# Optimization experiments

Measured on AMD Instinct MI355X. Metric: run time of the kernel, lower is better.

## Reference

```python
import jax, jax.numpy as jnp
import numpy as np

B, S, W, D, H = 2, 2048, 32, 1024, 16

def setup_inputs() -> dict:
    key = jax.random.key(0)
    ks = jax.random.split(key, 8)
    scale = 0.02
    return {
        'q': jax.random.normal(ks[0], (B, S, D), jnp.float32),
        'k': jax.random.normal(ks[1], (B, S, W, D), jnp.float32),
        'v': jax.random.normal(ks[2], (B, S, W, D), jnp.float32),
        'Wq': jax.random.normal(ks[3], (D, D), jnp.float32) * scale,
        'bq': jnp.zeros((D,), jnp.float32),
        'Wk': jax.random.normal(ks[4], (D, D), jnp.float32) * scale,
        'bk': jnp.zeros((D,), jnp.float32),
        'Wv': jax.random.normal(ks[5], (D, D), jnp.float32) * scale,
        'bv': jnp.zeros((D,), jnp.float32),
        'Wo': jax.random.normal(ks[6], (D, D), jnp.float32) * scale,
        'bo': jnp.zeros((D,), jnp.float32),
        'num_heads': H,
    }

def reference(q, k, v, Wq, bq, Wk, bk, Wv, bv, Wo, bo, num_heads):
    b, s, d = q.shape
    w = k.shape[2]
    hd = d // num_heads
    # query: Linear -> view(B,S,H,1,hd) -> transpose(1,2) => (B,H,S,1,hd)
    qh = (q @ Wq.T + bq).reshape(b, s, num_heads, 1, hd).transpose(0, 2, 1, 3, 4)
    # key/value: Linear then RAW view (B,H,S,W,hd) -- faithful to torch .view (no head transpose)
    kh = (k @ Wk.T + bk).reshape(b, num_heads, s, w, hd)
    vh = (v @ Wv.T + bv).reshape(b, num_heads, s, w, hd)
    # scores: (B,H,S,1,W), scaled by sqrt(head_dim) (query.shape[-1] inside attention)
    scores = jnp.einsum('bhsid,bhswd->bhsiw', qh, kh) / jnp.sqrt(jnp.float32(hd))
    # Softmax(dim=1) normalizes over the HEAD axis -- faithful to the original
    attn = jax.nn.softmax(scores, axis=1)
    A = jnp.einsum('bhsiw,bhswd->bhsid', attn, vh)[:, :, :, 0, :]  # (B,H,S,hd)
    out = A.reshape(b, s, d)  # raw view, matches torch .view(B,S,D)
    return out @ Wo.T + bo
```

## Files before the change

kernel.cpp:

```cpp
#include <hip/hip_runtime.h>
#include <hip/hip_bf16.h>


#define DEVI __device__ __forceinline__

typedef __attribute__((ext_vector_type(8))) short bf16x8;
typedef __attribute__((ext_vector_type(4))) float f32x4;
typedef const __attribute__((address_space(1))) void* gvp;
typedef __attribute__((address_space(3))) void* lvp;

DEVI ushort f2bf(float f) {
  uint u = __float_as_uint(f);
  u = u + 0x7fffu + ((u >> 16) & 1u);
  return (ushort)(u >> 16);
}
DEVI float bf2f(ushort u) { return __uint_as_float(((uint)u) << 16); }

__global__ __launch_bounds__(256) void cast_kernel(const float* __restrict__ in,
                                                   ushort* __restrict__ out,
                                                   long n) {
  long i = ((long)blockIdx.x * 256 + threadIdx.x) * 8;
  const long stride = (long)gridDim.x * 256 * 8;
  for (; i < n; i += stride) {
    float4 a = *reinterpret_cast<const float4*>(in + i);
    float4 b = *reinterpret_cast<const float4*>(in + i + 4);
    ushort o[8];
    o[0] = f2bf(a.x); o[1] = f2bf(a.y); o[2] = f2bf(a.z); o[3] = f2bf(a.w);
    o[4] = f2bf(b.x); o[5] = f2bf(b.y); o[6] = f2bf(b.z); o[7] = f2bf(b.w);
    *reinterpret_cast<int4*>(out + i) = *reinterpret_cast<const int4*>(o);
  }
}

template <int FJ0>
DEVI void mfma16b(f32x4 (&acc)[8][4], const bf16x8 (&A)[8], const bf16x8 (&B)[2]) {
  __builtin_amdgcn_s_setprio(1);
#pragma unroll
  for (int fi = 0; fi < 8; ++fi)
#pragma unroll
    for (int j = 0; j < 2; ++j)
      acc[fi][FJ0 + j] = __builtin_amdgcn_mfma_f32_16x16x32_bf16(
          A[fi], B[j], acc[fi][FJ0 + j], 0, 0, 0);
  __builtin_amdgcn_s_setprio(0);
}

__global__ __launch_bounds__(512)
__attribute__((amdgpu_waves_per_eu(2, 2)))
void gemm_big(const float* __restrict__ Ag, const ushort* __restrict__ Wg,
              const float* __restrict__ bias, ushort* __restrict__ Cg) {
  constexpr int K = 1024;
  __shared__ char lds[131072];
  const int tid = threadIdx.x;
  const int lane = tid & 63;
  const int wave = tid >> 6;
  const int wm = wave >> 2;
  const int wn = wave & 3;
  const int d = blockIdx.x;
  const int bn = (d >> 3) & 3;
  const size_t bm = (size_t)(d & 7) * (gridDim.x >> 5) + (d >> 5);

  const ushort* bB = Wg + (size_t)bn * 256 * K;

  const int r0 = tid >> 3;
  const int c0 = (tid & 7) ^ (r0 & 7);
  const float* pR0 = Ag + bm * 256 * K + (size_t)r0 * K + c0 * 8;
  const float* pR1 = pR0 + 64 * K;
  const ushort* bS0 = bB + (size_t)r0 * K + c0 * 8;
  const ushort* bS1 = bB + (size_t)(r0 + 64) * K + c0 * 8;
  const ushort* bS2 = bB + (size_t)(r0 + 128) * K + c0 * 8;
  const ushort* bS3 = bB + (size_t)(r0 + 192) * K + c0 * 8;

  const int lm = lane & 15;
  const int q = lane >> 4;
  const int rowB = lm * 128;
  const int swz0 = (q ^ (lm & 7)) * 16;
  const int swz1 = ((4 + q) ^ (lm & 7)) * 16;
  const char* ldsc = (const char*)lds;
  const char* p0A = ldsc + wm * 16384 + rowB;
  const char* p0B = ldsc + 32768 + (wn >> 1) * 16384 + (wn & 1) * 8192 + rowB;
  const char* p1A = p0A + 65536;
  const char* p1B = p0B + 65536;

  f32x4 acc[8][4] = {};
  bf16x8 A8[8];
  bf16x8 Bf[2];
  float4 st[8];

#define SB0 __builtin_amdgcn_sched_barrier(0)
#define BAR __builtin_amdgcn_s_barrier()
#define STG(p0, p1, ktE, ldsOff)                                                 \
  {                                                                              \
    __builtin_amdgcn_global_load_lds((gvp)((p0) + (ktE)),                        \
                                     (lvp)(lds + (ldsOff) + tid * 16), 16, 0, 0);\
    __builtin_amdgcn_global_load_lds((gvp)((p1) + (ktE)),                        \
                                     (lvp)(lds + (ldsOff) + 8192 + tid * 16),    \
                                     16, 0, 0);                                  \
  }
#define AISS8(off)                                                      \
  {                                                                     \
    st[0] = *reinterpret_cast<const float4*>(pR0 + (off));              \
    st[1] = *reinterpret_cast<const float4*>(pR0 + (off) + 4);          \
    st[2] = *reinterpret_cast<const float4*>(pR1 + (off));              \
    st[3] = *reinterpret_cast<const float4*>(pR1 + (off) + 4);          \
    st[4] = *reinterpret_cast<const float4*>(pR0 + 131072 + (off));     \
    st[5] = *reinterpret_cast<const float4*>(pR0 + 131072 + (off) + 4); \
    st[6] = *reinterpret_cast<const float4*>(pR1 + 131072 + (off));     \
    st[7] = *reinterpret_cast<const float4*>(pR1 + 131072 + (off) + 4); \
  }
#define CVTPAIR(v0, v1, dstoff)                                              \
  {                                                                          \
    uint w0, w1, w2, w3;                                                     \
    asm("v_cvt_pk_bf16_f32 %0,%1,%2" : "=v"(w0) : "v"((v0).x), "v"((v0).y)); \
    asm("v_cvt_pk_bf16_f32 %0,%1,%2" : "=v"(w1) : "v"((v0).z), "v"((v0).w)); \
    asm("v_cvt_pk_bf16_f32 %0,%1,%2" : "=v"(w2) : "v"((v1).x), "v"((v1).y)); \
    asm("v_cvt_pk_bf16_f32 %0,%1,%2" : "=v"(w3) : "v"((v1).z), "v"((v1).w)); \
    *reinterpret_cast<uint4*>(lds + (dstoff) + tid * 16) =                   \
        make_uint4(w0, w1, w2, w3);                                          \
  }
#define CVT8(base)                          \
  {                                         \
    CVTPAIR(st[0], st[1], (base));          \
    CVTPAIR(st[2], st[3], (base) + 8192);   \
    CVTPAIR(st[4], st[5], (base) + 16384);  \
    CVTPAIR(st[6], st[7], (base) + 24576);  \
  }
#define PH_SYNC()                                    \
  __builtin_amdgcn_s_barrier();                      \
  asm volatile("s_waitcnt lgkmcnt(0)" ::: "memory"); \
  SB0;
#define LDA8(p, swz)                                                       \
  _Pragma("unroll") for (int i_ = 0; i_ < 8; ++i_) {                       \
    A8[i_] = *reinterpret_cast<const bf16x8*>((p) + i_ * 2048 + (swz));    \
  }
#define LDB2(p, fjb, swz)                                                  \
  {                                                                        \
    Bf[0] = *reinterpret_cast<const bf16x8*>((p) + (fjb) + (swz));         \
    Bf[1] = *reinterpret_cast<const bf16x8*>((p) + (fjb) + 2048 + (swz));  \
  }

  AISS8(0); SB0;
  CVT8(0);
  SB0;
  STG(bS0, bS1, 0, 32768); STG(bS2, bS3, 0, 49152); SB0;
  AISS8(64); SB0;
  asm volatile("s_waitcnt vmcnt(8)" ::: "memory");
  asm volatile("s_waitcnt lgkmcnt(0)" ::: "memory");
  BAR;
  SB0;

#define ITER(M)                                                           \
  {                                                                       \
    const int ktB1 = (2 * it + 1) * 64;                                   \
    const int ktB2 = (2 * it + 2) * 64;                                   \
    const int ktA2 = (2 * it + 2) * 64;                                   \
    const int ktA3 = (2 * it + 3) * 64;                                   \
              \
    LDA8(p0A, swz0); LDB2(p0B, 0, swz0);                                  \
    STG(bS0, bS1, ktB1, 98304); STG(bS2, bS3, ktB1, 114688);              \
    PH_SYNC(); mfma16b<0>(acc, A8, Bf); BAR;                              \
        \
    LDB2(p0B, 4096, swz0);                                                \
    CVT8(65536);                                                          \
    SB0;                                                                  \
    if (M == 0) { AISS8(ktA2); SB0; }                                     \
    PH_SYNC(); mfma16b<2>(acc, A8, Bf); BAR;                              \
                                                  \
    LDA8(p0A, swz1); LDB2(p0B, 0, swz1);                                  \
    PH_SYNC(); mfma16b<0>(acc, A8, Bf); BAR;                              \
                   \
    LDB2(p0B, 4096, swz1);                                                \
    PH_SYNC(); mfma16b<2>(acc, A8, Bf);                                   \
    SB0;                                                                  \
    if (M == 0) { asm volatile("s_waitcnt vmcnt(8)" ::: "memory"); }      \
    else        { asm volatile("s_waitcnt vmcnt(0)" ::: "memory"); }      \
    BAR; SB0;                                                             \
              \
    LDA8(p1A, swz0); LDB2(p1B, 0, swz0);                                  \
    if (M == 0) { STG(bS0, bS1, ktB2, 32768); STG(bS2, bS3, ktB2, 49152); } \
    PH_SYNC(); mfma16b<0>(acc, A8, Bf); BAR;                              \
        \
    LDB2(p1B, 4096, swz0);                                                \
    if (M == 0) { CVT8(0); SB0; AISS8(ktA3); SB0; }                       \
    PH_SYNC(); mfma16b<2>(acc, A8, Bf); BAR;                              \
                                                  \
    LDA8(p1A, swz1); LDB2(p1B, 0, swz1);                                  \
    PH_SYNC(); mfma16b<0>(acc, A8, Bf); BAR;                              \
                   \
    LDB2(p1B, 4096, swz1);                                                \
    PH_SYNC(); mfma16b<2>(acc, A8, Bf);                                   \
    if (M == 0) {                                                         \
      SB0;                                                                \
      asm volatile("s_waitcnt vmcnt(8)" ::: "memory");                    \
      BAR; SB0;                                                           \
    }                                                                     \
  }

#pragma unroll 1
  for (int it = 0; it < 7; ++it) ITER(0);
  { const int it = 7; ITER(1); }
#undef ITER
#undef STG
#undef AISS8
#undef CVTPAIR
#undef CVT8
#undef PH_SYNC
#undef LDA8
#undef LDB2
#undef SB0
#undef BAR

#pragma unroll
  for (int fi = 0; fi < 8; ++fi) {
#pragma unroll
    for (int fj = 0; fj < 4; ++fj) {
      int n = bn * 256 + wn * 64 + fj * 16 + lm;
      float bv = bias[n];
#pragma unroll
      for (int r = 0; r < 4; ++r) {
        size_t m = bm * 256 + wm * 128 + fi * 16 + ((lane >> 4) * 4) + r;
        Cg[m * 1024 + n] = f2bf(acc[fi][fj][r] + bv);
      }
    }
  }
}

template <typename TOUT>
__global__ __launch_bounds__(256) void gemm_lds(const ushort* __restrict__ Ag,
                                                const ushort* __restrict__ Wg,
                                                const float* __restrict__ bias,
                                                TOUT* __restrict__ Cg) {
  constexpr int K = 1024;
  __shared__ ushort lA[128 * 64];
  __shared__ ushort lB[128 * 64];
  const int tid = threadIdx.x;
  const int lane = tid & 63;
  const int wave = tid >> 6;
  const int wr = (wave >> 1) * 64;
  const int wc = (wave & 1) * 64;
  const int d = blockIdx.x;
  const int bn = (d >> 3) & 7;
  const size_t bm = (size_t)(d & 7) * (gridDim.x >> 6) + (d >> 6);

  const ushort* aB = Ag + bm * 128 * K;
  const ushort* bB = Wg + (size_t)bn * 128 * K;
  const int srow = wave * 32 + (lane >> 3);
  const int scol = ((lane & 7) ^ (lane >> 3)) * 8;
  char* lAc = (char*)lA;
  char* lBc = (char*)lB;

  f32x4 acc[4][4] = {};

  for (int kt = 0; kt < K; kt += 64) {
    __syncthreads();
#pragma unroll
    for (int c = 0; c < 4; ++c) {
      __builtin_amdgcn_global_load_lds(
          (gvp)(aB + (size_t)(srow + c * 8) * K + kt + scol),
          (lvp)(lAc + wave * 4096 + c * 1024), 16, 0, 0);
      __builtin_amdgcn_global_load_lds(
          (gvp)(bB + (size_t)(srow + c * 8) * K + kt + scol),
          (lvp)(lBc + wave * 4096 + c * 1024), 16, 0, 0);
    }
    __syncthreads();
#pragma unroll
    for (int kk = 0; kk < 2; ++kk) {
      bf16x8 af[4], bg[4];
#pragma unroll
      for (int fi = 0; fi < 4; ++fi) {
        int r = wr + fi * 16 + (lane & 15);
        int byte = (r * 128 + kk * 64 + ((lane >> 4) * 16)) ^ ((r & 7) << 4);
        af[fi] = *reinterpret_cast<const bf16x8*>(lAc + byte);
      }
#pragma unroll
      for (int fj = 0; fj < 4; ++fj) {
        int r = wc + fj * 16 + (lane & 15);
        int byte = (r * 128 + kk * 64 + ((lane >> 4) * 16)) ^ ((r & 7) << 4);
        bg[fj] = *reinterpret_cast<const bf16x8*>(lBc + byte);
      }
#pragma unroll
      for (int fi = 0; fi < 4; ++fi)
#pragma unroll
        for (int fj = 0; fj < 4; ++fj)
          acc[fi][fj] = __builtin_amdgcn_mfma_f32_16x16x32_bf16(af[fi], bg[fj],
                                                                acc[fi][fj], 0, 0, 0);
    }
  }
#pragma unroll
  for (int fi = 0; fi < 4; ++fi) {
#pragma unroll
    for (int fj = 0; fj < 4; ++fj) {
      int n = bn * 128 + wc + fj * 16 + (lane & 15);
      float bv = bias[n];
#pragma unroll
      for (int r = 0; r < 4; ++r) {
        size_t m = bm * 128 + wr + fi * 16 + ((lane >> 4) * 4) + r;
        float val = acc[fi][fj][r] + bv;
        if constexpr (sizeof(TOUT) == 2)
          reinterpret_cast<ushort*>(Cg)[m * 1024 + n] = f2bf(val);
        else
          reinterpret_cast<float*>(Cg)[m * 1024 + n] = val;
      }
    }
  }
}

template <typename TIN, typename TOUT>
__global__ __launch_bounds__(256) void gemm_bias(const TIN* __restrict__ Ag,
                                                 const float* __restrict__ Wg,
                                                 const float* __restrict__ bias,
                                                 TOUT* __restrict__ Cg) {
  constexpr int K = 1024;
  __shared__ char lA[128 * 64 * 2];
  __shared__ char lB[128 * 64 * 2];
  const int tid = threadIdx.x;
  const int lane = tid & 63;
  const int wave = tid >> 6;
  const int wr = (wave >> 1) * 64;
  const int wc = (wave & 1) * 64;
  const int bn = blockIdx.x;
  const size_t bm = blockIdx.y;

  const TIN* aBase = Ag + bm * 128 * K;
  const float* bBase = Wg + (size_t)bn * 128 * K;

  f32x4 acc[4][4] = {};

  for (int kt = 0; kt < K; kt += 64) {
    __syncthreads();
    if constexpr (sizeof(TIN) == 4) {
#pragma unroll
      for (int i = 0; i < 8; ++i) {
        int f = tid + i * 256;
        int row = f >> 4, c4 = f & 15;
        const float4 v = *reinterpret_cast<const float4*>(
            reinterpret_cast<const float*>(aBase) + (size_t)row * K + kt + c4 * 4);
        ushort4 pk;
        pk.x = f2bf(v.x); pk.y = f2bf(v.y); pk.z = f2bf(v.z); pk.w = f2bf(v.w);
        int byte = (row * 128 + c4 * 8) ^ ((row & 7) << 4);
        *reinterpret_cast<ushort4*>(lA + byte) = pk;
      }
    } else {
#pragma unroll
      for (int i = 0; i < 4; ++i) {
        int f = tid + i * 256;
        int row = f >> 3, c8 = f & 7;
        int4 v = *reinterpret_cast<const int4*>(
            reinterpret_cast<const ushort*>(aBase) + (size_t)row * K + kt + c8 * 8);
        int byte = (row * 128 + c8 * 16) ^ ((row & 7) << 4);
        *reinterpret_cast<int4*>(lA + byte) = v;
      }
    }
#pragma unroll
    for (int i = 0; i < 8; ++i) {
      int f = tid + i * 256;
      int row = f >> 4, c4 = f & 15;
      const float4 v =
          *reinterpret_cast<const float4*>(bBase + (size_t)row * K + kt + c4 * 4);
      ushort4 pk;
      pk.x = f2bf(v.x); pk.y = f2bf(v.y); pk.z = f2bf(v.z); pk.w = f2bf(v.w);
      int byte = (row * 128 + c4 * 8) ^ ((row & 7) << 4);
      *reinterpret_cast<ushort4*>(lB + byte) = pk;
    }
    __syncthreads();
#pragma unroll
    for (int kk = 0; kk < 2; ++kk) {
      bf16x8 af[4], bg[4];
#pragma unroll
      for (int fi = 0; fi < 4; ++fi) {
        int r = wr + fi * 16 + (lane & 15);
        int byte = (r * 128 + kk * 64 + ((lane >> 4) * 16)) ^ ((r & 7) << 4);
        af[fi] = *reinterpret_cast<const bf16x8*>(lA + byte);
      }
#pragma unroll
      for (int fj = 0; fj < 4; ++fj) {
        int r = wc + fj * 16 + (lane & 15);
        int byte = (r * 128 + kk * 64 + ((lane >> 4) * 16)) ^ ((r & 7) << 4);
        bg[fj] = *reinterpret_cast<const bf16x8*>(lB + byte);
      }
#pragma unroll
      for (int fi = 0; fi < 4; ++fi)
#pragma unroll
        for (int fj = 0; fj < 4; ++fj)
          acc[fi][fj] =
              __builtin_amdgcn_mfma_f32_16x16x32_bf16(af[fi], bg[fj], acc[fi][fj], 0, 0, 0);
    }
  }
#pragma unroll
  for (int fi = 0; fi < 4; ++fi) {
#pragma unroll
    for (int fj = 0; fj < 4; ++fj) {
      int n = bn * 128 + wc + fj * 16 + (lane & 15);
      float bv = bias[n];
#pragma unroll
      for (int r = 0; r < 4; ++r) {
        size_t m = bm * 128 + wr + fi * 16 + ((lane >> 4) * 4) + r;
        float val = acc[fi][fj][r] + bv;
        if constexpr (sizeof(TOUT) == 2)
          reinterpret_cast<ushort*>(Cg)[m * 1024 + n] = f2bf(val);
        else
          reinterpret_cast<float*>(Cg)[m * 1024 + n] = val;
      }
    }
  }
}

__global__ __launch_bounds__(512) void attn_kernel(const ushort* __restrict__ Q,
                                                   const ushort* __restrict__ Kl,
                                                   const ushort* __restrict__ Vl,
                                                   ushort* __restrict__ Aout) {
  const int bs = blockIdx.x;
  const int b = bs >> 11, sp = bs & 2047;
  const int tid = threadIdx.x;
  const int wave = tid >> 6, lane = tid & 63;

  __shared__ ushort qrow[1024];
  __shared__ float sc[16][32];
  __shared__ float attnw[16][32];
  __shared__ float mx[32], rinv[32];

  reinterpret_cast<uint*>(qrow)[tid] =
      reinterpret_cast<const uint*>(Q + (size_t)bs * 1024)[tid];
  __syncthreads();

  const int wp = lane & 31, half = lane >> 5;
#pragma unroll
  for (int hh = 0; hh < 2; ++hh) {
    const int h = wave * 2 + hh;
    const int s_k = h * 128 + (sp >> 4);
    const int w_k = (sp & 15) * 2 + (wp >> 4);
    const ushort* kp =
        Kl + (((size_t)(b * 2048 + s_k) * 32) + w_k) * 1024 + (wp & 15) * 64 + half * 32;
    const ushort* qp = qrow + h * 64 + half * 32;
    float dot = 0.f;
#pragma unroll
    for (int j = 0; j < 32; j += 8) {
      int4 kv = *reinterpret_cast<const int4*>(kp + j);
      int4 qv = *reinterpret_cast<const int4*>(qp + j);
      const ushort* ka = reinterpret_cast<const ushort*>(&kv);
      const ushort* qa = reinterpret_cast<const ushort*>(&qv);
#pragma unroll
      for (int t = 0; t < 8; ++t) dot += bf2f(ka[t]) * bf2f(qa[t]);
    }
    dot += __shfl_xor(dot, 32);
    if (half == 0) sc[h][wp] = dot * 0.125f;
  }
  __syncthreads();
  if (tid < 32) {
    float m = sc[0][tid];
#pragma unroll
    for (int h = 1; h < 16; ++h) m = fmaxf(m, sc[h][tid]);
    float s = 0.f;
#pragma unroll
    for (int h = 0; h < 16; ++h) s += __expf(sc[h][tid] - m);
    mx[tid] = m;
    rinv[tid] = 1.f / s;
  }
  __syncthreads();
  if (lane < 32) {
#pragma unroll
    for (int hh = 0; hh < 2; ++hh) {
      const int h = wave * 2 + hh;
      attnw[h][lane] = __expf(sc[h][lane] - mx[lane]) * rinv[lane];
    }
  }
  __syncthreads();
#pragma unroll
  for (int hh = 0; hh < 2; ++hh) {
    const int h = wave * 2 + hh;
    const int s_k = h * 128 + (sp >> 4);
    const size_t vb = (((size_t)(b * 2048 + s_k) * 32) + (sp & 15) * 2) * 1024;
    float a = 0.f;
#pragma unroll
    for (int w2 = 0; w2 < 32; ++w2) {
      float wgt = attnw[h][w2];
      a += wgt * bf2f(Vl[vb + (size_t)(w2 >> 4) * 1024 + (w2 & 15) * 64 + lane]);
    }
    Aout[(((size_t)(b * 16 + h)) * 2048 + sp) * 64 + lane] = f2bf(a);
  }
}

extern "C" void kernel_launch(void* const* d_in, const int* in_sizes, int n_in,
                              void* d_out, int out_size, void* d_ws, size_t ws_size,
                              hipStream_t stream) {
  const float* q = (const float*)d_in[0];
  const float* k = (const float*)d_in[1];
  const float* v = (const float*)d_in[2];
  const float* Wq = (const float*)d_in[3];
  const float* bq = (const float*)d_in[4];
  const float* Wk = (const float*)d_in[5];
  const float* bk = (const float*)d_in[6];
  const float* Wv = (const float*)d_in[7];
  const float* bv = (const float*)d_in[8];
  const float* Wo = (const float*)d_in[9];
  const float* bo = (const float*)d_in[10];
  float* out = (float*)d_out;

  char* ws = (char*)d_ws;
  const size_t MB = 1u << 20;
  ushort* Qlin = (ushort*)ws;
  ushort* Aws  = (ushort*)(ws + 8 * MB);
  ushort* wkbf = (ushort*)(ws + 16 * MB);
  ushort* wvbf = (ushort*)(ws + 18 * MB);
  ushort* wqbf = (ushort*)(ws + 20 * MB);
  ushort* wobf = (ushort*)(ws + 22 * MB);
  ushort* qbf  = (ushort*)(ws + 24 * MB);
  ushort* Klin = (ushort*)(ws + 32 * MB);
  ushort* Vlin = (ushort*)(ws + 288 * MB);
  const bool full = ws_size >= 800 * MB;

  if (full) {
    cast_kernel<<<dim3(512), 256, 0, stream>>>(Wq, wqbf, 1048576L);
    cast_kernel<<<dim3(512), 256, 0, stream>>>(Wk, wkbf, 1048576L);
    cast_kernel<<<dim3(512), 256, 0, stream>>>(Wv, wvbf, 1048576L);
    cast_kernel<<<dim3(512), 256, 0, stream>>>(Wo, wobf, 1048576L);
    cast_kernel<<<dim3(2048), 256, 0, stream>>>(q, qbf, 4194304L);
    gemm_lds<ushort><<<dim3(256), 256, 0, stream>>>(qbf, wqbf, bq, Qlin);
    gemm_big<<<dim3(2048), 512, 0, stream>>>(k, wkbf, bk, Klin);
    gemm_big<<<dim3(2048), 512, 0, stream>>>(v, wvbf, bv, Vlin);
    attn_kernel<<<dim3(4096), dim3(512), 0, stream>>>(Qlin, Klin, Vlin, Aws);
    gemm_lds<float><<<dim3(256), 256, 0, stream>>>(Aws, wobf, bo, out);
  } else {
    gemm_bias<float, ushort><<<dim3(8, 32), 256, 0, stream>>>(q, Wq, bq, Qlin);
    gemm_bias<float, ushort><<<dim3(8, 1024), 256, 0, stream>>>(k, Wk, bk, Klin);
    gemm_bias<float, ushort><<<dim3(8, 1024), 256, 0, stream>>>(v, Wv, bv, Vlin);
    attn_kernel<<<dim3(4096), dim3(512), 0, stream>>>(Qlin, Klin, Vlin, Aws);
    gemm_bias<ushort, float><<<dim3(8, 32), 256, 0, stream>>>(Aws, Wo, bo, out);
  }
}
```

Baseline: 913.7 us.

## Fuse V fp32-to-bf16 cast into K projection GEMM, add bf16-input V GEMM

The K projection GEMM now also streams the fp32 V tensor, converting it to bf16 in slots between its MFMA phases and writing it to a workspace buffer. A new bf16-input GEMM with a 4-slot global_load_lds pipeline then computes the V projection from that buffer. The aim is to hide V's conversion cost under the compute-bound K GEMM and let the V GEMM read half the bytes. The price is extra bf16 write and read traffic for V, plus added memory and register pressure inside the K GEMM's carefully scheduled loop.

```diff
diff --git a/kernel.cpp b/kernel.cpp
--- a/kernel.cpp
+++ b/kernel.cpp
@@ -45,8 +45,9 @@
 
 __global__ __launch_bounds__(512)
 __attribute__((amdgpu_waves_per_eu(2, 2)))
-void gemm_big(const float* __restrict__ Ag, const ushort* __restrict__ Wg,
-              const float* __restrict__ bias, ushort* __restrict__ Cg) {
+void gemm_big_f32(const float* __restrict__ Ag, const ushort* __restrict__ Wg,
+                  const float* __restrict__ bias, ushort* __restrict__ Cg,
+                  const float* __restrict__ Vsrc, ushort* __restrict__ Vbf) {
   constexpr int K = 1024;
   __shared__ char lds[131072];
   const int tid = threadIdx.x;
@@ -80,10 +81,14 @@
   const char* p1A = p0A + 65536;
   const char* p1B = p0B + 65536;
 
+  const float* rsrc = Vsrc + (size_t)d * 65536 + tid * 4;
+  ushort* rdst = Vbf + (size_t)d * 65536 + tid * 4;
+
   f32x4 acc[8][4] = {};
   bf16x8 A8[8];
   bf16x8 Bf[2];
   float4 st[8];
+  float4 rv;
 
 #define SB0 __builtin_amdgcn_sched_barrier(0)
 #define BAR __builtin_amdgcn_s_barrier()
@@ -136,6 +141,14 @@
     Bf[0] = *reinterpret_cast<const bf16x8*>((p) + (fjb) + (swz));         \
     Bf[1] = *reinterpret_cast<const bf16x8*>((p) + (fjb) + 2048 + (swz));  \
   }
+#define RLD(u) { rv = *reinterpret_cast<const float4*>(rsrc + (size_t)(u) * 2048); }
+#define RST(u)                                                               \
+  {                                                                          \
+    uint w0, w1;                                                             \
+    asm("v_cvt_pk_bf16_f32 %0,%1,%2" : "=v"(w0) : "v"(rv.x), "v"(rv.y));     \
+    asm("v_cvt_pk_bf16_f32 %0,%1,%2" : "=v"(w1) : "v"(rv.z), "v"(rv.w));     \
+    *reinterpret_cast<uint2*>(rdst + (size_t)(u) * 2048) = make_uint2(w0, w1);\
+  }
 
   AISS8(0); SB0;
   CVT8(0);
@@ -156,18 +169,22 @@
               \
     LDA8(p0A, swz0); LDB2(p0B, 0, swz0);                                  \
     STG(bS0, bS1, ktB1, 98304); STG(bS2, bS3, ktB1, 114688);              \
+    RLD(it * 4 + 0);                                                      \
     PH_SYNC(); mfma16b<0>(acc, A8, Bf); BAR;                              \
         \
     LDB2(p0B, 4096, swz0);                                                \
     CVT8(65536);                                                          \
     SB0;                                                                  \
     if (M == 0) { AISS8(ktA2); SB0; }                                     \
+    RST(it * 4 + 0);                                                      \
     PH_SYNC(); mfma16b<2>(acc, A8, Bf); BAR;                              \
                                                   \
     LDA8(p0A, swz1); LDB2(p0B, 0, swz1);                                  \
+    RLD(it * 4 + 1);                                                      \
     PH_SYNC(); mfma16b<0>(acc, A8, Bf); BAR;                              \
                    \
     LDB2(p0B, 4096, swz1);                                                \
+    RST(it * 4 + 1);                                                      \
     PH_SYNC(); mfma16b<2>(acc, A8, Bf);                                   \
     SB0;                                                                  \
     if (M == 0) { asm volatile("s_waitcnt vmcnt(8)" ::: "memory"); }      \
@@ -176,16 +193,20 @@
               \
     LDA8(p1A, swz0); LDB2(p1B, 0, swz0);                                  \
     if (M == 0) { STG(bS0, bS1, ktB2, 32768); STG(bS2, bS3, ktB2, 49152); } \
+    RLD(it * 4 + 2);                                                      \
     PH_SYNC(); mfma16b<0>(acc, A8, Bf); BAR;                              \
         \
     LDB2(p1B, 4096, swz0);                                                \
     if (M == 0) { CVT8(0); SB0; AISS8(ktA3); SB0; }                       \
+    RST(it * 4 + 2);                                                      \
     PH_SYNC(); mfma16b<2>(acc, A8, Bf); BAR;                              \
                                                   \
     LDA8(p1A, swz1); LDB2(p1B, 0, swz1);                                  \
+    RLD(it * 4 + 3);                                                      \
     PH_SYNC(); mfma16b<0>(acc, A8, Bf); BAR;                              \
                    \
     LDB2(p1B, 4096, swz1);                                                \
+    RST(it * 4 + 3);                                                      \
     PH_SYNC(); mfma16b<2>(acc, A8, Bf);                                   \
     if (M == 0) {                                                         \
       SB0;                                                                \
@@ -205,8 +226,120 @@
 #undef PH_SYNC
 #undef LDA8
 #undef LDB2
+#undef RLD
+#undef RST
 #undef SB0
 #undef BAR
+
+#pragma unroll
+  for (int fi = 0; fi < 8; ++fi) {
+#pragma unroll
+    for (int fj = 0; fj < 4; ++fj) {
+      int n = bn * 256 + wn * 64 + fj * 16 + lm;
+      float bv = bias[n];
+#pragma unroll
+      for (int r = 0; r < 4; ++r) {
+        size_t m = bm * 256 + wm * 128 + fi * 16 + ((lane >> 4) * 4) + r;
+        Cg[m * 1024 + n] = f2bf(acc[fi][fj][r] + bv);
+      }
+    }
+  }
+}
+
+__global__ __launch_bounds__(512, 2) void gemm_big_bf16(const ushort* __restrict__ Ag,
+                                                        const ushort* __restrict__ Wg,
+                                                        const float* __restrict__ bias,
+                                                        ushort* __restrict__ Cg) {
+  constexpr int K = 1024;
+  constexpr int NT = 32;
+  constexpr int SLOT = 32768;
+  __shared__ char lds[4 * SLOT];
+  const int tid = threadIdx.x;
+  const int lane = tid & 63;
+  const int wave = tid >> 6;
+  const int wm = wave >> 2;
+  const int wn = wave & 3;
+  const int d = blockIdx.x;
+  const int bn = (d >> 3) & 3;
+  const size_t bm = (size_t)(d & 7) * (gridDim.x >> 5) + (d >> 5);
+
+  const ushort* aB = Ag + bm * 256 * K;
+  const ushort* bB = Wg + (size_t)bn * 256 * K;
+
+  const int ar0 = tid >> 2, ac0 = (tid & 3) ^ ((ar0 >> 1) & 3);
+  const int ar1 = (tid + 512) >> 2, ac1 = (tid & 3) ^ ((ar1 >> 1) & 3);
+  const ushort* aS0 = aB + (size_t)ar0 * K + ac0 * 8;
+  const ushort* aS1 = aB + (size_t)ar1 * K + ac1 * 8;
+  const ushort* bS0 = bB + (size_t)ar0 * K + ac0 * 8;
+  const ushort* bS1 = bB + (size_t)ar1 * K + ac1 * 8;
+  const int adst0 = tid * 16;
+  const int adst1 = tid * 16 + 8192;
+  const int bdst0 = 16384 + tid * 16;
+  const int bdst1 = 24576 + tid * 16;
+
+  const int lm = lane & 15;
+  const int cs = (lm >> 1) & 3;
+  const int cSwz = ((lane >> 4) ^ cs) * 16;
+  const int offA = lm * 64 + cSwz + wm * 8192;
+  const int offB = 16384 + lm * 64 + cSwz + wn * 4096;
+
+  f32x4 acc[8][4] = {};
+
+#define STAGE_T(slotOff, ktElem)                                                   \
+  {                                                                                \
+    __builtin_amdgcn_global_load_lds((gvp)(aS0 + (ktElem)),                        \
+                                     (lvp)(lds + (slotOff) + adst0), 16, 0, 0);    \
+    __builtin_amdgcn_global_load_lds((gvp)(aS1 + (ktElem)),                        \
+                                     (lvp)(lds + (slotOff) + adst1), 16, 0, 0);    \
+    __builtin_amdgcn_global_load_lds((gvp)(bS0 + (ktElem)),                        \
+                                     (lvp)(lds + (slotOff) + bdst0), 16, 0, 0);    \
+    __builtin_amdgcn_global_load_lds((gvp)(bS1 + (ktElem)),                        \
+                                     (lvp)(lds + (slotOff) + bdst1), 16, 0, 0);    \
+  }
+
+  STAGE_T(0 * SLOT, 0);
+  STAGE_T(1 * SLOT, 32);
+  STAGE_T(2 * SLOT, 64);
+  __builtin_amdgcn_sched_barrier(0);
+  asm volatile("s_waitcnt vmcnt(8)" ::: "memory");
+  __builtin_amdgcn_s_barrier();
+  __builtin_amdgcn_sched_barrier(0);
+
+  int rdOff = 0, stOff = 3 * SLOT;
+  for (int t = 0; t < NT; ++t) {
+    if (t + 3 < NT) STAGE_T(stOff, (t + 3) * 32);
+    const char* pA = (const char*)lds + rdOff + offA;
+    const char* pB = (const char*)lds + rdOff + offB;
+    bf16x8 a[8], b[4];
+#pragma unroll
+    for (int fi = 0; fi < 8; ++fi)
+      a[fi] = *reinterpret_cast<const bf16x8*>(pA + fi * 1024);
+#pragma unroll
+    for (int fj = 0; fj < 4; ++fj)
+      b[fj] = *reinterpret_cast<const bf16x8*>(pB + fj * 1024);
+    __builtin_amdgcn_s_setprio(1);
+#pragma unroll
+    for (int fi = 0; fi < 8; ++fi)
+#pragma unroll
+      for (int fj = 0; fj < 4; ++fj)
+        acc[fi][fj] = __builtin_amdgcn_mfma_f32_16x16x32_bf16(a[fi], b[fj],
+                                                              acc[fi][fj], 0, 0, 0);
+    __builtin_amdgcn_s_setprio(0);
+    if (t < NT - 1) {
+      __builtin_amdgcn_sched_barrier(0);
+      if (t <= NT - 4)
+        asm volatile("s_waitcnt vmcnt(8)" ::: "memory");
+      else if (t == NT - 3)
+        asm volatile("s_waitcnt vmcnt(4)" ::: "memory");
+      else
+        asm volatile("s_waitcnt vmcnt(0)" ::: "memory");
+      __builtin_amdgcn_s_barrier();
+      __builtin_amdgcn_sched_barrier(0);
+    }
+    rdOff = (rdOff == 3 * SLOT) ? 0 : rdOff + SLOT;
+    stOff = (stOff == 3 * SLOT) ? 0 : stOff + SLOT;
+  }
+#undef STAGE_T
 
 #pragma unroll
   for (int fi = 0; fi < 8; ++fi) {
@@ -505,6 +638,7 @@
   ushort* qbf  = (ushort*)(ws + 24 * MB);
   ushort* Klin = (ushort*)(ws + 32 * MB);
   ushort* Vlin = (ushort*)(ws + 288 * MB);
+  ushort* vbf  = (ushort*)(ws + 544 * MB);
   const bool full = ws_size >= 800 * MB;
 
   if (full) {
@@ -514,8 +648,8 @@
     cast_kernel<<<dim3(512), 256, 0, stream>>>(Wo, wobf, 1048576L);
     cast_kernel<<<dim3(2048), 256, 0, stream>>>(q, qbf, 4194304L);
     gemm_lds<ushort><<<dim3(256), 256, 0, stream>>>(qbf, wqbf, bq, Qlin);
-    gemm_big<<<dim3(2048), 512, 0, stream>>>(k, wkbf, bk, Klin);
-    gemm_big<<<dim3(2048), 512, 0, stream>>>(v, wvbf, bv, Vlin);
+    gemm_big_f32<<<dim3(2048), 512, 0, stream>>>(k, wkbf, bk, Klin, v, vbf);
+    gemm_big_bf16<<<dim3(2048), 512, 0, stream>>>(vbf, wvbf, bv, Vlin);
     attn_kernel<<<dim3(4096), dim3(512), 0, stream>>>(Qlin, Klin, Vlin, Aws);
     gemm_lds<float><<<dim3(256), 256, 0, stream>>>(Aws, wobf, bo, out);
   } else {
```

Measured after the change: 954.9 us. 4.5% more time.
